# Performance work log

Measured on AMD Instinct MI355X. Metric: run time of the kernel, lower is better.

## Reference

```python
import jax, jax.numpy as jnp
import numpy as np

EPS = 1e-5

def _layernorm(x, w, b):
    # x: [B, L, C]; WithBias_LayerNorm over last dim (biased variance)
    mu = jnp.mean(x, axis=-1, keepdims=True)
    var = jnp.mean((x - mu) ** 2, axis=-1, keepdims=True)
    return (x - mu) / jnp.sqrt(var + EPS) * w + b

def _selective_scan(x, x_proj_w, dt_w, A_logs, Ds):
    # x: [B, D, L]  (D = ssm d_inner = 192, N = d_state = 16, R = dt_rank = 6)
    Bsz, D, L = x.shape
    N = A_logs.shape[1]
    R = dt_w.shape[1]
    x_dbl = jnp.einsum('bdl,rd->blr', x, x_proj_w)            # [B, L, R+2N]
    dts_r = x_dbl[..., :R]
    Bs = x_dbl[..., R:R + N]                                   # [B, L, N]
    Cs = x_dbl[..., R + N:]                                    # [B, L, N]
    dts = jax.nn.softplus(jnp.einsum('blr,dr->bld', dts_r, dt_w))  # [B, L, D]
    As = -jnp.exp(A_logs.astype(jnp.float32))                  # [D, N]
    dt_A = jnp.exp(jnp.einsum('bld,dn->bldn', dts, As))        # [B, L, D, N]
    dt_B_x = jnp.einsum('bld,bln,bdl->bldn', dts, Bs, x)       # [B, L, D, N]

    def step(u, inp):
        a, bx, c = inp                                         # [B,D,N],[B,D,N],[B,N]
        u = a * u + bx
        y = jnp.einsum('bdn,bn->bd', u, c)
        return u, y

    u0 = jnp.zeros((Bsz, D, N), dtype=jnp.float32)
    _, ys = jax.lax.scan(step, u0, (jnp.swapaxes(dt_A, 0, 1),
                                     jnp.swapaxes(dt_B_x, 0, 1),
                                     jnp.swapaxes(Cs, 0, 1)))
    y = jnp.swapaxes(ys, 0, 1)                                 # [B, L, D]
    y = y + jnp.einsum('bdl,d->bld', x, Ds.astype(jnp.float32))
    return y


def setup_inputs() -> dict:
    key = jax.random.key(0)
    ks = jax.random.split(key, 12)
    B, C, H, W = 64, 2048, 24, 8
    D_in2, Dssm, N, R = 384, 192, 16, 6
    s = 0.02
    return {
        'feat_map': jax.random.normal(ks[0], (B, C, H, W), jnp.float32),
        'ln_w': jnp.ones((C,), jnp.float32),
        'ln_b': jnp.zeros((C,), jnp.float32),
        'in_w': jax.random.normal(ks[1], (D_in2, C), jnp.float32) * s,
        'in_b': jnp.zeros((D_in2,), jnp.float32),
        'x_proj_w': jax.random.normal(ks[2], (R + 2 * N, Dssm), jnp.float32) * s,
        'dt_w': jax.random.normal(ks[3], (Dssm, R), jnp.float32) * 0.1,
        'A_logs': jnp.log(jnp.broadcast_to(jnp.arange(1, N + 1, dtype=jnp.float32), (Dssm, N))),
        'Ds': jnp.ones((Dssm,), jnp.float32),
        'out_w': jax.random.normal(ks[4], (C, Dssm), jnp.float32) * s,
        'out_b': jnp.zeros((C,), jnp.float32),
        'mo_w': jax.random.normal(ks[5], (C, C), jnp.float32) * s,
        'mo_b': jnp.zeros((C,), jnp.float32),
        'bn_w': jnp.ones((C,), jnp.float32),
        'bn_b': jnp.zeros((C,), jnp.float32),
        'bn_rm': jax.random.normal(ks[6], (C,), jnp.float32) * 0.1,
        'bn_rv': jax.random.uniform(ks[7], (C,), jnp.float32) + 0.5,
    }


def reference(feat_map, ln_w, ln_b, in_w, in_b, x_proj_w, dt_w, A_logs, Ds,
              out_w, out_b, mo_w, mo_b, bn_w, bn_b, bn_rm, bn_rv):
    B, C, H, W = feat_map.shape
    L = H * W
    x3 = feat_map.transpose(0, 2, 3, 1).reshape(B, L, C)       # to_3d
    fm = _layernorm(x3, ln_w, ln_b)                            # normalized feat_map [B, L, C]
    xz = jnp.einsum('blc,oc->blo', fm, in_w) + in_b            # 1x1 conv in_proj
    x, z = jnp.split(xz, 2, axis=-1)                           # each [B, L, 192]
    xd = jnp.swapaxes(x, 1, 2)                                 # [B, D, L]
    yf = _selective_scan(xd, x_proj_w, dt_w, A_logs, Ds)       # [B, L, D]
    yb = _selective_scan(xd[:, :, ::-1], x_proj_w, dt_w, A_logs, Ds)[:, ::-1, :]
    ssm = yf + yb                                              # [B, L, D]
    ssm = ssm * jax.nn.silu(z)
    out = jnp.einsum('bld,cd->blc', ssm, out_w) + out_b        # out_proj 1x1 conv
    out = out + fm                                             # drop_path is identity at eval
    out = jnp.einsum('blc,oc->blo', out, mo_w) + mo_b          # mamba_out conv 1x1
    out = (out - bn_rm) / jnp.sqrt(bn_rv + EPS) * bn_w + bn_b  # BatchNorm (eval)
    out = jax.nn.relu(out)
    return out.reshape(B, H, W, C).transpose(0, 3, 1, 2)
```

## Files before the change

kernel.cpp:

```cpp
#include <hip/hip_runtime.h>
#include <math.h>

#define EPSV 1e-5f


typedef __attribute__((ext_vector_type(8))) __bf16 bf16x8;
typedef __attribute__((ext_vector_type(4))) float f32x4;

__device__ __forceinline__ ushort f2bf(float f) {
  union { float f; unsigned u; } v; v.f = f;
  const unsigned r = v.u + 0x7fffu + ((v.u >> 16) & 1u);
  return (ushort)(r >> 16);
}

#define GLOAD16(G, L) __builtin_amdgcn_global_load_lds( \
    (__attribute__((address_space(1))) void*)(G), \
    (__attribute__((address_space(3))) void*)(L), 16, 0, 0)

__global__ __launch_bounds__(256) void cvt_kernel(
    const float* __restrict__ s, ushort* __restrict__ d, int n)
{
  const int i = (blockIdx.x * 256 + threadIdx.x) * 4;
  if (i + 3 < n) {
    const float4 v = *(const float4*)(s + i);
    ushort4 o;
    o.x = f2bf(v.x); o.y = f2bf(v.y); o.z = f2bf(v.z); o.w = f2bf(v.w);
    *(ushort4*)(d + i) = o;
  }
}

__global__ __launch_bounds__(256) void transpose_w(
    const float* __restrict__ w, ushort* __restrict__ wT)
{
  __shared__ float t[64][65];
  const int c0 = blockIdx.x * 64, d0 = blockIdx.y * 64;
  const int tl = threadIdx.x & 63, tg = threadIdx.x >> 6;
#pragma unroll
  for (int r = 0; r < 16; ++r) {
    const int c = r * 4 + tg;
    t[c][tl] = w[(size_t)(c0 + c) * 192 + d0 + tl];
  }
  __syncthreads();
#pragma unroll
  for (int r = 0; r < 16; ++r) {
    const int d = r * 4 + tg;
    wT[(size_t)(d0 + d) * 2048 + c0 + tl] = f2bf(t[tl][d]);
  }
}

__global__ __launch_bounds__(256) void ln_stats(
    const float* __restrict__ feat, float* __restrict__ sums)
{
  const int b = blockIdx.x, c0 = blockIdx.y * 128;
  const int l = threadIdx.x;
  if (l >= 192) return;
  const float* p = feat + ((size_t)b * 2048 + c0) * 192 + l;
  float s = 0.f, sq = 0.f;
  for (int c = 0; c < 128; ++c) { const float v = p[(size_t)c * 192]; s += v; sq = fmaf(v, v, sq); }
  atomicAdd(&sums[(b * 192 + l) * 2], s);
  atomicAdd(&sums[(b * 192 + l) * 2 + 1], sq);
}

__global__ __launch_bounds__(256) void ln_apply(
    const float* __restrict__ feat, const float* __restrict__ sums,
    const float* __restrict__ lnw, const float* __restrict__ lnb,
    ushort* __restrict__ fm)
{
  __shared__ float tile[64][65];
  __shared__ float smu[64], srs[64];
  const int b = blockIdx.x, c0 = blockIdx.y * 64, l0 = blockIdx.z * 64;
  const int tl = threadIdx.x & 63, tg = threadIdx.x >> 6;
#pragma unroll
  for (int r = 0; r < 16; ++r) {
    const int c = r * 4 + tg;
    tile[c][tl] = feat[((size_t)b * 2048 + c0 + c) * 192 + l0 + tl];
  }
  if (threadIdx.x < 64) {
    const float s  = sums[(b * 192 + l0 + threadIdx.x) * 2];
    const float sq = sums[(b * 192 + l0 + threadIdx.x) * 2 + 1];
    const float mu = s * (1.f / 2048.f);
    smu[threadIdx.x] = mu;
    srs[threadIdx.x] = rsqrtf(sq * (1.f / 2048.f) - mu * mu + EPSV);
  }
  __syncthreads();
  const float w = lnw[c0 + tl], bb = lnb[c0 + tl];
#pragma unroll
  for (int r = 0; r < 16; ++r) {
    const int ll = r * 4 + tg;
    fm[((size_t)(b * 192 + l0 + ll)) * 2048 + c0 + tl] =
        f2bf((tile[tl][ll] - smu[ll]) * srs[ll] * w + bb);
  }
}

__device__ __forceinline__ void mfma_phase(
    const ushort* __restrict__ Ag, int lda,
    const ushort* __restrict__ Bg, int ldb, int K,
    int bm, int bn, int tid, ushort* As, ushort* Bs, f32x4 acc[4][4])
{
  const int lane = tid & 63, wave = tid >> 6;
  const int wm = (wave & 1) << 6, wn = (wave >> 1) << 6;
  const int fr = lane & 15, q = lane >> 4;
  const int r0 = tid >> 2, kc = (tid & 3) << 3;
  const int lb = (tid & 192) * 8;
  for (int k0 = 0; k0 < K; k0 += 32) {
    __syncthreads();
    GLOAD16(Ag + (size_t)(bm + r0) * lda + k0 + kc,      As + lb);
    GLOAD16(Ag + (size_t)(bm + 64 + r0) * lda + k0 + kc, As + 2048 + lb);
    GLOAD16(Bg + (size_t)(bn + r0) * ldb + k0 + kc,      Bs + lb);
    GLOAD16(Bg + (size_t)(bn + 64 + r0) * ldb + k0 + kc, Bs + 2048 + lb);
    __syncthreads();
    bf16x8 af[4], bfr[4];
#pragma unroll
    for (int i = 0; i < 4; ++i) {
      af[i]  = *(const bf16x8*)&As[(wm + i * 16 + fr) * 32 + q * 8];
      bfr[i] = *(const bf16x8*)&Bs[(wn + i * 16 + fr) * 32 + q * 8];
    }
#pragma unroll
    for (int i = 0; i < 4; ++i)
#pragma unroll
      for (int j = 0; j < 4; ++j)
        acc[i][j] = __builtin_amdgcn_mfma_f32_16x16x32_bf16(af[i], bfr[j], acc[i][j], 0, 0, 0);
  }
}

template<int MODE>
__global__ __launch_bounds__(256) void mfma_gemm(
    const ushort* __restrict__ A1, const ushort* __restrict__ B1,
    const ushort* __restrict__ A2, const ushort* __restrict__ B2,
    const float* __restrict__ p0, const float* __restrict__ p1,
    float* __restrict__ out, ushort* __restrict__ outb)
{
  __shared__ ushort As[4096], Bs[4096];
  const int tid = threadIdx.x;
  const int bm = blockIdx.y * 128, bn = blockIdx.x * 128;
  f32x4 acc[4][4];
#pragma unroll
  for (int i = 0; i < 4; ++i)
#pragma unroll
    for (int j = 0; j < 4; ++j) acc[i][j] = (f32x4)(0.f);

  mfma_phase(A1, 2048, B1, 2048, 2048, bm, bn, tid, As, Bs, acc);
  if (MODE == 1)
    mfma_phase(A2, 192, B2, 192, 192, bm, bn, tid, As, Bs, acc);

  const int lane = tid & 63, wave = tid >> 6;
  const int wm = (wave & 1) << 6, wn = (wave >> 1) << 6;
  const int fr = lane & 15, q = lane >> 4;
  if (MODE == 0) {
#pragma unroll
    for (int mi = 0; mi < 4; ++mi) {
      const int m0 = bm + wm + mi * 16 + q * 4;
#pragma unroll
      for (int ni = 0; ni < 4; ++ni) {
        const int n = bn + wn + ni * 16 + fr;
        const float bias = p0[n];
#pragma unroll
        for (int r = 0; r < 4; ++r)
          out[(size_t)(m0 + r) * 384 + n] = acc[mi][ni][r] + bias;
      }
    }
  } else if (MODE == 1) {
#pragma unroll
    for (int mi = 0; mi < 4; ++mi) {
      const int m0 = bm + wm + mi * 16 + q * 4;
      const int b = m0 / 192, l0 = m0 - b * 192;
#pragma unroll
      for (int ni = 0; ni < 4; ++ni) {
        const int n = bn + wn + ni * 16 + fr;
        const float sc = p0[n], sh = p1[n];
        float4 o;
        o.x = fmaxf(fmaf(acc[mi][ni][0], sc, sh), 0.f);
        o.y = fmaxf(fmaf(acc[mi][ni][1], sc, sh), 0.f);
        o.z = fmaxf(fmaf(acc[mi][ni][2], sc, sh), 0.f);
        o.w = fmaxf(fmaf(acc[mi][ni][3], sc, sh), 0.f);
        *(float4*)(out + ((size_t)b * 2048 + n) * 192 + l0) = o;
      }
    }
  } else {
#pragma unroll
    for (int mi = 0; mi < 4; ++mi) {
      const int m0 = bm + wm + mi * 16 + q * 4;
#pragma unroll
      for (int ni = 0; ni < 4; ++ni) {
        const int n = bn + wn + ni * 16 + fr;
        if (n < 192) {
#pragma unroll
          for (int r = 0; r < 4; ++r)
            outb[(size_t)(m0 + r) * 192 + n] = f2bf(acc[mi][ni][r]);
        }
      }
    }
  }
}

__global__ __launch_bounds__(64) void xproj_kernel(
    const float* __restrict__ xz, const float* __restrict__ xpw,
    const float* __restrict__ dtw, float* __restrict__ dts,
    float* __restrict__ Bsb, float* __restrict__ Csb)
{
  const int m = blockIdx.x, tid = threadIdx.x;
  __shared__ float xrow[192];
  __shared__ float xdbl[38];
  const float* src = xz + (size_t)m * 384;
#pragma unroll
  for (int i = 0; i < 3; ++i) xrow[tid + i * 64] = src[tid + i * 64];
  __syncthreads();
  if (tid < 38) {
    float a = 0.f;
    const float* wr = xpw + tid * 192;
    for (int d = 0; d < 192; ++d) a = fmaf(xrow[d], wr[d], a);
    xdbl[tid] = a;
  }
  __syncthreads();
  if (tid < 16) Bsb[(size_t)m * 16 + tid] = xdbl[6 + tid];
  else if (tid < 32) Csb[(size_t)m * 16 + (tid - 16)] = xdbl[22 + (tid - 16)];
#pragma unroll
  for (int i = 0; i < 3; ++i) {
    const int d = tid + i * 64;
    const float* w = dtw + d * 6;
    float a = xdbl[0] * w[0] + xdbl[1] * w[1] + xdbl[2] * w[2]
            + xdbl[3] * w[3] + xdbl[4] * w[4] + xdbl[5] * w[5];
    dts[(size_t)m * 192 + d] = (a > 20.f) ? a : log1pf(__expf(a));
  }
}

__global__ __launch_bounds__(256) void scan_kernel(
    const float* __restrict__ xz, const float* __restrict__ dts,
    const float* __restrict__ Bsb, const float* __restrict__ Csb,
    const float* __restrict__ A_logs, const float* __restrict__ Ds,
    ushort* __restrict__ ssm)
{
  __shared__ float s_dt[3072], s_x[3072], s_B[3072], s_C[3072], s_y[3072];
  const int tid = threadIdx.x;
  const int b = blockIdx.x / 12, dblk = blockIdx.x - b * 12;
  const int d0 = dblk * 16;
  const size_t rbase = (size_t)b * 192;
  for (int i = tid; i < 768; i += 256) {
    const int l = i >> 2, j = (i & 3) << 2;
    const size_t row = rbase + l;
    ((float4*)s_dt)[i] = *(const float4*)(dts + row * 192 + d0 + j);
    ((float4*)s_x)[i]  = *(const float4*)(xz  + row * 384 + d0 + j);
    ((float4*)s_B)[i]  = *(const float4*)(Bsb + row * 16 + j);
    ((float4*)s_C)[i]  = *(const float4*)(Csb + row * 16 + j);
  }
  __syncthreads();
  const int n = tid & 15, dl = tid >> 4;
  const float Acoef = -expf(A_logs[(d0 + dl) * 16 + n]);
  float u = 0.f;
#pragma unroll 4
  for (int l = 0; l < 192; ++l) {
    const float dt = s_dt[l * 16 + dl];
    const float c  = dt * s_B[l * 16 + n] * s_x[l * 16 + dl];
    const float a  = __expf(dt * Acoef);
    u = fmaf(a, u, c);
    float y = u * s_C[l * 16 + n];
    y += __shfl_xor(y, 1, 16); y += __shfl_xor(y, 2, 16);
    y += __shfl_xor(y, 4, 16); y += __shfl_xor(y, 8, 16);
    if (n == 0) s_y[l * 16 + dl] = y;
  }
  u = 0.f;
#pragma unroll 4
  for (int l = 191; l >= 0; --l) {
    const float dt = s_dt[l * 16 + dl];
    const float c  = dt * s_B[l * 16 + n] * s_x[l * 16 + dl];
    const float a  = __expf(dt * Acoef);
    u = fmaf(a, u, c);
    float y = u * s_C[l * 16 + n];
    y += __shfl_xor(y, 1, 16); y += __shfl_xor(y, 2, 16);
    y += __shfl_xor(y, 4, 16); y += __shfl_xor(y, 8, 16);
    if (n == 0) s_y[l * 16 + dl] += y;
  }
  __syncthreads();
  for (int i = tid; i < 768; i += 256) {
    const int l = i >> 2, j = (i & 3) << 2;
    const size_t row = rbase + l;
    const float4 y4 = ((const float4*)s_y)[i];
    const float4 x4 = ((const float4*)s_x)[i];
    const float4 z4 = *(const float4*)(xz + row * 384 + 192 + d0 + j);
    const float4 D4 = *(const float4*)(Ds + d0 + j);
    ushort4 o;
    o.x = f2bf((y4.x + 2.f * x4.x * D4.x) * (z4.x / (1.f + __expf(-z4.x))));
    o.y = f2bf((y4.y + 2.f * x4.y * D4.y) * (z4.y / (1.f + __expf(-z4.y))));
    o.z = f2bf((y4.z + 2.f * x4.z * D4.z) * (z4.z / (1.f + __expf(-z4.z))));
    o.w = f2bf((y4.w + 2.f * x4.w * D4.w) * (z4.w / (1.f + __expf(-z4.w))));
    *(ushort4*)(ssm + row * 192 + d0 + j) = o;
  }
}

__global__ __launch_bounds__(64) void prep_kernel(
    const float* __restrict__ mo_w, const float* __restrict__ mo_b,
    const float* __restrict__ out_b,
    const float* __restrict__ bn_w, const float* __restrict__ bn_b,
    const float* __restrict__ bn_rm, const float* __restrict__ bn_rv,
    float* __restrict__ scale, float* __restrict__ shift)
{
  const int o = blockIdx.x, tid = threadIdx.x;
  float s = 0.f;
  for (int c = tid; c < 2048; c += 64) s = fmaf(mo_w[(size_t)o * 2048 + c], out_b[c], s);
#pragma unroll
  for (int off = 32; off > 0; off >>= 1) s += __shfl_down(s, off, 64);
  if (tid == 0) {
    const float b2 = s + mo_b[o];
    const float sc = bn_w[o] * rsqrtf(bn_rv[o] + EPSV);
    scale[o] = sc;
    shift[o] = (b2 - bn_rm[o]) * sc + bn_b[o];
  }
}

extern "C" void kernel_launch(void* const* d_in, const int* in_sizes, int n_in,
                              void* d_out, int out_size, void* d_ws, size_t ws_size,
                              hipStream_t stream) {
  const float* feat  = (const float*)d_in[0];
  const float* ln_w  = (const float*)d_in[1];
  const float* ln_b  = (const float*)d_in[2];
  const float* in_w  = (const float*)d_in[3];
  const float* in_b  = (const float*)d_in[4];
  const float* xpw   = (const float*)d_in[5];
  const float* dtw   = (const float*)d_in[6];
  const float* A_logs= (const float*)d_in[7];
  const float* Ds    = (const float*)d_in[8];
  const float* out_w = (const float*)d_in[9];
  const float* out_b = (const float*)d_in[10];
  const float* mo_w  = (const float*)d_in[11];
  const float* mo_b  = (const float*)d_in[12];
  const float* bn_w  = (const float*)d_in[13];
  const float* bn_b  = (const float*)d_in[14];
  const float* bn_rm = (const float*)d_in[15];
  const float* bn_rv = (const float*)d_in[16];
  float* out = (float*)d_out;

  uint8_t* p = (uint8_t*)d_ws;
  ushort* fm_b  = (ushort*)p; p += (size_t)12288 * 2048 * 2;
  float*  xz    = (float*)p;  p += (size_t)12288 * 384 * 4;
  float*  dts   = (float*)p;  p += (size_t)12288 * 192 * 4;
  float*  Bsb   = (float*)p;  p += (size_t)12288 * 16 * 4;
  float*  Csb   = (float*)p;  p += (size_t)12288 * 16 * 4;
  ushort* ssm_b = (ushort*)p; p += (size_t)12288 * 192 * 2;
  ushort* W2b   = (ushort*)p; p += (size_t)2048 * 192 * 2;
  ushort* owT_b = (ushort*)p; p += (size_t)256 * 2048 * 2;
  ushort* mo_wb = (ushort*)p; p += (size_t)2048 * 2048 * 2;
  ushort* in_wb = (ushort*)p; p += (size_t)384 * 2048 * 2;
  float*  scale = (float*)p;  p += 2048 * 4;
  float*  shift = (float*)p;  p += 2048 * 4;
  float*  sums  = (float*)p;  p += (size_t)64 * 192 * 2 * 4;
  if ((size_t)(p - (uint8_t*)d_ws) > ws_size) return;

  cvt_kernel<<<4096, 256, 0, stream>>>(mo_w, mo_wb, 2048 * 2048);
  cvt_kernel<<<768, 256, 0, stream>>>(in_w, in_wb, 384 * 2048);
  hipMemsetAsync(owT_b, 0, (size_t)256 * 2048 * 2, stream);
  transpose_w<<<dim3(32, 3), 256, 0, stream>>>(out_w, owT_b);

  hipMemsetAsync(sums, 0, (size_t)64 * 192 * 2 * 4, stream);
  ln_stats<<<dim3(64, 16), 256, 0, stream>>>(feat, sums);
  ln_apply<<<dim3(64, 32, 3), 256, 0, stream>>>(feat, sums, ln_w, ln_b, fm_b);

  mfma_gemm<0><<<dim3(3, 96), 256, 0, stream>>>(
      fm_b, in_wb, nullptr, nullptr, in_b, nullptr, xz, nullptr);

  xproj_kernel<<<12288, 64, 0, stream>>>(xz, xpw, dtw, dts, Bsb, Csb);
  scan_kernel<<<768, 256, 0, stream>>>(xz, dts, Bsb, Csb, A_logs, Ds, ssm_b);

  mfma_gemm<2><<<dim3(2, 16), 256, 0, stream>>>(
      mo_wb, owT_b, nullptr, nullptr, nullptr, nullptr, nullptr, W2b);
  prep_kernel<<<2048, 64, 0, stream>>>(mo_w, mo_b, out_b, bn_w, bn_b, bn_rm, bn_rv, scale, shift);

  mfma_gemm<1><<<dim3(16, 96), 256, 0, stream>>>(
      fm_b, mo_wb, ssm_b, W2b, scale, shift, out, nullptr);
}
```

Before: 720.2 us.

## Split-K small GEMMs with atomics, remap blocks across XCDs, batch xproj rows

The in_proj GEMM (288 blocks) and the weight-fold GEMM (32 blocks) are split along K into 4 and 8 chunks, accumulating into zeroed fp32 buffers with atomicAdd. This raises block counts so all CUs are used. The in_proj bias moves into the xproj and scan kernels, and the folded weight gets an extra conversion to bf16. The main GEMM uses a 1D grid remapped so consecutive M tiles land on the same XCD for L2 reuse of the A rows, and xproj now handles 4 rows per 256-thread block. The cost is memsets, atomic traffic and an extra conversion pass.

```diff
diff --git a/kernel.cpp b/kernel.cpp
--- a/kernel.cpp
+++ b/kernel.cpp
@@ -94,7 +94,7 @@
 
 __device__ __forceinline__ void mfma_phase(
     const ushort* __restrict__ Ag, int lda,
-    const ushort* __restrict__ Bg, int ldb, int K,
+    const ushort* __restrict__ Bg, int ldb, int kbeg, int kend,
     int bm, int bn, int tid, ushort* As, ushort* Bs, f32x4 acc[4][4])
 {
   const int lane = tid & 63, wave = tid >> 6;
@@ -102,7 +102,7 @@
   const int fr = lane & 15, q = lane >> 4;
   const int r0 = tid >> 2, kc = (tid & 3) << 3;
   const int lb = (tid & 192) * 8;
-  for (int k0 = 0; k0 < K; k0 += 32) {
+  for (int k0 = kbeg; k0 < kend; k0 += 32) {
     __syncthreads();
     GLOAD16(Ag + (size_t)(bm + r0) * lda + k0 + kc,      As + lb);
     GLOAD16(Ag + (size_t)(bm + 64 + r0) * lda + k0 + kc, As + 2048 + lb);
@@ -128,20 +128,38 @@
     const ushort* __restrict__ A1, const ushort* __restrict__ B1,
     const ushort* __restrict__ A2, const ushort* __restrict__ B2,
     const float* __restrict__ p0, const float* __restrict__ p1,
-    float* __restrict__ out, ushort* __restrict__ outb)
+    float* __restrict__ out)
 {
   __shared__ ushort As[4096], Bs[4096];
   const int tid = threadIdx.x;
-  const int bm = blockIdx.y * 128, bn = blockIdx.x * 128;
+  const int bidx = blockIdx.x;
+  int bm, bn;
   f32x4 acc[4][4];
 #pragma unroll
   for (int i = 0; i < 4; ++i)
 #pragma unroll
     for (int j = 0; j < 4; ++j) acc[i][j] = (f32x4)(0.f);
 
-  mfma_phase(A1, 2048, B1, 2048, 2048, bm, bn, tid, As, Bs, acc);
-  if (MODE == 1)
-    mfma_phase(A2, 192, B2, 192, 192, bm, bn, tid, As, Bs, acc);
+  if (MODE == 0) {
+    const int xcd = bidx & 7, j = bidx >> 3;
+    bm = (xcd * 12 + j % 12) * 128;
+    const int t = j / 12;
+    bn = (t % 3) * 128;
+    const int kz = t / 3;
+    mfma_phase(A1, 2048, B1, 2048, kz * 512, kz * 512 + 512, bm, bn, tid, As, Bs, acc);
+  } else if (MODE == 1) {
+    const int xcd = bidx & 7, j = bidx >> 3;
+    bm = (xcd * 12 + j % 12) * 128;
+    bn = (j / 12) * 128;
+    mfma_phase(A1, 2048, B1, 2048, 0, 2048, bm, bn, tid, As, Bs, acc);
+    mfma_phase(A2, 192, B2, 192, 0, 192, bm, bn, tid, As, Bs, acc);
+  } else {
+    bn = (bidx & 1) * 128;
+    const int r = bidx >> 1;
+    bm = (r & 15) * 128;
+    const int kz = r >> 4;
+    mfma_phase(A1, 2048, B1, 2048, kz * 256, kz * 256 + 256, bm, bn, tid, As, Bs, acc);
+  }
 
   const int lane = tid & 63, wave = tid >> 6;
   const int wm = (wave & 1) << 6, wn = (wave >> 1) << 6;
@@ -153,10 +171,9 @@
 #pragma unroll
       for (int ni = 0; ni < 4; ++ni) {
         const int n = bn + wn + ni * 16 + fr;
-        const float bias = p0[n];
 #pragma unroll
         for (int r = 0; r < 4; ++r)
-          out[(size_t)(m0 + r) * 384 + n] = acc[mi][ni][r] + bias;
+          atomicAdd(&out[(size_t)(m0 + r) * 384 + n], acc[mi][ni][r]);
       }
     }
   } else if (MODE == 1) {
@@ -186,46 +203,52 @@
         if (n < 192) {
 #pragma unroll
           for (int r = 0; r < 4; ++r)
-            outb[(size_t)(m0 + r) * 192 + n] = f2bf(acc[mi][ni][r]);
+            atomicAdd(&out[(size_t)(m0 + r) * 192 + n], acc[mi][ni][r]);
         }
       }
     }
   }
 }
 
-__global__ __launch_bounds__(64) void xproj_kernel(
-    const float* __restrict__ xz, const float* __restrict__ xpw,
-    const float* __restrict__ dtw, float* __restrict__ dts,
-    float* __restrict__ Bsb, float* __restrict__ Csb)
-{
-  const int m = blockIdx.x, tid = threadIdx.x;
-  __shared__ float xrow[192];
-  __shared__ float xdbl[38];
+__global__ __launch_bounds__(256) void xproj_kernel(
+    const float* __restrict__ xz, const float* __restrict__ in_b,
+    const float* __restrict__ xpw, const float* __restrict__ dtw,
+    float* __restrict__ dts, float* __restrict__ Bsb, float* __restrict__ Csb)
+{
+  __shared__ float xrow[4][192];
+  __shared__ float xdbl[4][38];
+  const int tid = threadIdx.x;
+  const int r = tid >> 6, lane = tid & 63;
+  const int m = blockIdx.x * 4 + r;
   const float* src = xz + (size_t)m * 384;
 #pragma unroll
-  for (int i = 0; i < 3; ++i) xrow[tid + i * 64] = src[tid + i * 64];
-  __syncthreads();
-  if (tid < 38) {
+  for (int i = 0; i < 3; ++i) {
+    const int c = lane + i * 64;
+    xrow[r][c] = src[c] + in_b[c];
+  }
+  __syncthreads();
+  if (lane < 38) {
     float a = 0.f;
-    const float* wr = xpw + tid * 192;
-    for (int d = 0; d < 192; ++d) a = fmaf(xrow[d], wr[d], a);
-    xdbl[tid] = a;
-  }
-  __syncthreads();
-  if (tid < 16) Bsb[(size_t)m * 16 + tid] = xdbl[6 + tid];
-  else if (tid < 32) Csb[(size_t)m * 16 + (tid - 16)] = xdbl[22 + (tid - 16)];
+    const float* wr = xpw + lane * 192;
+    for (int d = 0; d < 192; ++d) a = fmaf(xrow[r][d], wr[d], a);
+    xdbl[r][lane] = a;
+  }
+  __syncthreads();
+  if (lane < 16) Bsb[(size_t)m * 16 + lane] = xdbl[r][6 + lane];
+  else if (lane < 32) Csb[(size_t)m * 16 + (lane - 16)] = xdbl[r][22 + (lane - 16)];
 #pragma unroll
   for (int i = 0; i < 3; ++i) {
-    const int d = tid + i * 64;
+    const int d = lane + i * 64;
     const float* w = dtw + d * 6;
-    float a = xdbl[0] * w[0] + xdbl[1] * w[1] + xdbl[2] * w[2]
-            + xdbl[3] * w[3] + xdbl[4] * w[4] + xdbl[5] * w[5];
+    float a = xdbl[r][0] * w[0] + xdbl[r][1] * w[1] + xdbl[r][2] * w[2]
+            + xdbl[r][3] * w[3] + xdbl[r][4] * w[4] + xdbl[r][5] * w[5];
     dts[(size_t)m * 192 + d] = (a > 20.f) ? a : log1pf(__expf(a));
   }
 }
 
 __global__ __launch_bounds__(256) void scan_kernel(
-    const float* __restrict__ xz, const float* __restrict__ dts,
+    const float* __restrict__ xz, const float* __restrict__ in_b,
+    const float* __restrict__ dts,
     const float* __restrict__ Bsb, const float* __restrict__ Csb,
     const float* __restrict__ A_logs, const float* __restrict__ Ds,
     ushort* __restrict__ ssm)
@@ -239,9 +262,13 @@
     const int l = i >> 2, j = (i & 3) << 2;
     const size_t row = rbase + l;
     ((float4*)s_dt)[i] = *(const float4*)(dts + row * 192 + d0 + j);
-    ((float4*)s_x)[i]  = *(const float4*)(xz  + row * 384 + d0 + j);
-    ((float4*)s_B)[i]  = *(const float4*)(Bsb + row * 16 + j);
-    ((float4*)s_C)[i]  = *(const float4*)(Csb + row * 16 + j);
+    const float4 xv = *(const float4*)(xz + row * 384 + d0 + j);
+    const float4 bi = *(const float4*)(in_b + d0 + j);
+    float4 sx; sx.x = xv.x + bi.x; sx.y = xv.y + bi.y;
+    sx.z = xv.z + bi.z; sx.w = xv.w + bi.w;
+    ((float4*)s_x)[i] = sx;
+    ((float4*)s_B)[i] = *(const float4*)(Bsb + row * 16 + j);
+    ((float4*)s_C)[i] = *(const float4*)(Csb + row * 16 + j);
   }
   __syncthreads();
   const int n = tid & 15, dl = tid >> 4;
@@ -276,8 +303,11 @@
     const size_t row = rbase + l;
     const float4 y4 = ((const float4*)s_y)[i];
     const float4 x4 = ((const float4*)s_x)[i];
-    const float4 z4 = *(const float4*)(xz + row * 384 + 192 + d0 + j);
+    const float4 zr = *(const float4*)(xz + row * 384 + 192 + d0 + j);
+    const float4 bz = *(const float4*)(in_b + 192 + d0 + j);
     const float4 D4 = *(const float4*)(Ds + d0 + j);
+    float4 z4; z4.x = zr.x + bz.x; z4.y = zr.y + bz.y;
+    z4.z = zr.z + bz.z; z4.w = zr.w + bz.w;
     ushort4 o;
     o.x = f2bf((y4.x + 2.f * x4.x * D4.x) * (z4.x / (1.f + __expf(-z4.x))));
     o.y = f2bf((y4.y + 2.f * x4.y * D4.y) * (z4.y / (1.f + __expf(-z4.y))));
@@ -336,6 +366,7 @@
   float*  Bsb   = (float*)p;  p += (size_t)12288 * 16 * 4;
   float*  Csb   = (float*)p;  p += (size_t)12288 * 16 * 4;
   ushort* ssm_b = (ushort*)p; p += (size_t)12288 * 192 * 2;
+  float*  W2f   = (float*)p;  p += (size_t)2048 * 192 * 4;
   ushort* W2b   = (ushort*)p; p += (size_t)2048 * 192 * 2;
   ushort* owT_b = (ushort*)p; p += (size_t)256 * 2048 * 2;
   ushort* mo_wb = (ushort*)p; p += (size_t)2048 * 2048 * 2;
@@ -354,16 +385,19 @@
   ln_stats<<<dim3(64, 16), 256, 0, stream>>>(feat, sums);
   ln_apply<<<dim3(64, 32, 3), 256, 0, stream>>>(feat, sums, ln_w, ln_b, fm_b);
 
-  mfma_gemm<0><<<dim3(3, 96), 256, 0, stream>>>(
-      fm_b, in_wb, nullptr, nullptr, in_b, nullptr, xz, nullptr);
-
-  xproj_kernel<<<12288, 64, 0, stream>>>(xz, xpw, dtw, dts, Bsb, Csb);
-  scan_kernel<<<768, 256, 0, stream>>>(xz, dts, Bsb, Csb, A_logs, Ds, ssm_b);
-
-  mfma_gemm<2><<<dim3(2, 16), 256, 0, stream>>>(
-      mo_wb, owT_b, nullptr, nullptr, nullptr, nullptr, nullptr, W2b);
+  hipMemsetAsync(xz, 0, (size_t)12288 * 384 * 4, stream);
+  mfma_gemm<0><<<1152, 256, 0, stream>>>(
+      fm_b, in_wb, nullptr, nullptr, nullptr, nullptr, xz);
+
+  xproj_kernel<<<3072, 256, 0, stream>>>(xz, in_b, xpw, dtw, dts, Bsb, Csb);
+  scan_kernel<<<768, 256, 0, stream>>>(xz, in_b, dts, Bsb, Csb, A_logs, Ds, ssm_b);
+
+  hipMemsetAsync(W2f, 0, (size_t)2048 * 192 * 4, stream);
+  mfma_gemm<2><<<256, 256, 0, stream>>>(
+      mo_wb, owT_b, nullptr, nullptr, nullptr, nullptr, W2f);
+  cvt_kernel<<<384, 256, 0, stream>>>(W2f, W2b, 2048 * 192);
   prep_kernel<<<2048, 64, 0, stream>>>(mo_w, mo_b, out_b, bn_w, bn_b, bn_rm, bn_rv, scale, shift);
 
-  mfma_gemm<1><<<dim3(16, 96), 256, 0, stream>>>(
-      fm_b, mo_wb, ssm_b, W2b, scale, shift, out, nullptr);
-}
+  mfma_gemm<1><<<1536, 256, 0, stream>>>(
+      fm_b, mo_wb, ssm_b, W2b, scale, shift, out);
+}
```

Result: slower. 742.4 us (+3.1%).
